# Performance work log

Hardware: AMD Instinct MI355X
Metric: run time of the kernel (lower is better)

The kernel has to match this reference:

```python
import jax, jax.numpy as jnp
import numpy as np


def setup_inputs() -> dict:
    key = jax.random.key(0)
    k1, k2 = jax.random.split(key)
    B, L, D = 8, 4096, 1024
    hidden_states = jax.random.normal(k1, (B, L, D), dtype=jnp.float32)
    token_mask = jax.random.bernoulli(k2, 0.5, (B, L))
    return {"hidden_states": hidden_states, "token_mask": token_mask}


def reference(hidden_states, token_mask):
    """Compact hidden states at masked positions, left-packed and zero-padded.

    Returns (chunked: (B, M, D), counts: (B,)) where M = max tokens per row.
    Vectorized: prefix-sum over the mask gives per-row scatter destinations;
    masked-out positions are routed to a scratch slot M that is sliced off.
    """
    B, L, D = hidden_states.shape
    counts = token_mask.sum(axis=1).astype(jnp.int32)  # (B,)
    M = int(jnp.max(counts))  # data-dependent pad width (eager, matches .item())
    if M == 0:
        return hidden_states[:, :0, :], counts
    # destination index within each row: 0..count-1 for kept tokens, M for dropped
    dest = jnp.where(token_mask, jnp.cumsum(token_mask, axis=1) - 1, M)  # (B, L)
    b_idx = jnp.arange(B)[:, None]  # (B, 1)
    out = jnp.zeros((B, M + 1, D), hidden_states.dtype)
    out = out.at[b_idx, dest].set(hidden_states)  # single fused scatter
    chunked = out[:, :M, :]  # drop scratch slot
    return chunked, counts
```

## Files before the change

kernel.cpp:

```cpp
#include <hip/hip_runtime.h>
#include <hip/hip_bf16.h>


__global__ void scan_kernel(const int* __restrict__ mask,
                            int* __restrict__ src_idx,
                            int* __restrict__ counts_ws,
                            float* __restrict__ counts_out,
                            int L, int M) {
    const int b = blockIdx.x;
    const int t = threadIdx.x;
    const int nthreads = blockDim.x;
    const int per = L / nthreads;
    const int* row = mask + (size_t)b * L;
    const int base = t * per;

    int s = 0;
    for (int i = 0; i < per; ++i) s += (row[base + i] != 0);

    __shared__ int sums[256];
    sums[t] = s;
    __syncthreads();

    for (int off = 1; off < nthreads; off <<= 1) {
        int v = (t >= off) ? sums[t - off] : 0;
        __syncthreads();
        sums[t] += v;
        __syncthreads();
    }

    const int total = sums[nthreads - 1];
    int prefix = (t == 0) ? 0 : sums[t - 1];

    int* srow = src_idx + (size_t)b * M;
    for (int i = 0; i < per; ++i) {
        if (row[base + i] != 0) {
            srow[prefix] = base + i;
            ++prefix;
        }
    }

    if (t == 0) {
        counts_ws[b] = total;
        counts_out[b] = (float)total;
    }
}

__global__ void pack_kernel(const float4* __restrict__ hidden,
                            const int* __restrict__ src_idx,
                            const int* __restrict__ counts,
                            float4* __restrict__ out,
                            int L, int M, int D4) {
    const int m = blockIdx.x;
    const int b = blockIdx.y;
    const size_t orow = ((size_t)b * M + m) * D4;

    if (m < counts[b]) {
        const int l = src_idx[(size_t)b * M + m];
        const size_t irow = ((size_t)b * L + l) * D4;
        for (int t = threadIdx.x; t < D4; t += blockDim.x)
            out[orow + t] = hidden[irow + t];
    } else {
        const float4 z = make_float4(0.f, 0.f, 0.f, 0.f);
        for (int t = threadIdx.x; t < D4; t += blockDim.x)
            out[orow + t] = z;
    }
}

extern "C" void kernel_launch(void* const* d_in, const int* in_sizes, int n_in,
                              void* d_out, int out_size, void* d_ws, size_t ws_size,
                              hipStream_t stream) {
    const int B = 8;
    const int BL = in_sizes[1];
    const int D  = in_sizes[0] / BL;
    const int L  = BL / B;
    const int M  = (out_size - B) / (B * D);

    const float* hidden = (const float*)d_in[0];
    const int*   mask   = (const int*)d_in[1];
    float*       out    = (float*)d_out;

    int* counts_ws = (int*)d_ws;
    int* src_idx   = (int*)d_ws + 64;

    float* counts_out = out + (size_t)B * M * D;

    scan_kernel<<<B, 256, 0, stream>>>(mask, src_idx, counts_ws, counts_out, L, M);

    if (M > 0) {
        dim3 grid(M, B);
        pack_kernel<<<grid, 256, 0, stream>>>((const float4*)hidden, src_idx,
                                              counts_ws, (float4*)out, L, M, D / 4);
    }
}
```

Before: 205.1 us.

## Use wave-shuffle scan with 1024 threads and grid-stride persistent pack kernel

```diff
diff --git a/kernel.cpp b/kernel.cpp
--- a/kernel.cpp
+++ b/kernel.cpp
@@ -2,67 +2,73 @@
 #include <hip/hip_bf16.h>
 
 
-__global__ void scan_kernel(const int* __restrict__ mask,
-                            int* __restrict__ src_idx,
-                            int* __restrict__ counts_ws,
-                            float* __restrict__ counts_out,
-                            int L, int M) {
+__global__ __launch_bounds__(1024) void scan_kernel(
+        const int* __restrict__ mask,
+        int* __restrict__ src_idx,
+        int* __restrict__ counts_ws,
+        float* __restrict__ counts_out,
+        int L, int M) {
     const int b = blockIdx.x;
     const int t = threadIdx.x;
-    const int nthreads = blockDim.x;
-    const int per = L / nthreads;
-    const int* row = mask + (size_t)b * L;
-    const int base = t * per;
+    const int lane = t & 63;
+    const int wid  = t >> 6;
+    const int base = t * 4;
 
-    int s = 0;
-    for (int i = 0; i < per; ++i) s += (row[base + i] != 0);
+    const int4 v = *(const int4*)(mask + (size_t)b * L + base);
+    const int m0 = (v.x != 0), m1 = (v.y != 0), m2 = (v.z != 0), m3 = (v.w != 0);
+    const int s = m0 + m1 + m2 + m3;
 
-    __shared__ int sums[256];
-    sums[t] = s;
+    int incl = s;
+    #pragma unroll
+    for (int off = 1; off < 64; off <<= 1) {
+        int up = __shfl_up(incl, off, 64);
+        if (lane >= off) incl += up;
+    }
+
+    __shared__ int wsum[16];
+    __shared__ int wexc[17];
+    if (lane == 63) wsum[wid] = incl;
+    __syncthreads();
+    if (t == 0) {
+        int acc = 0;
+        #pragma unroll
+        for (int w = 0; w < 16; ++w) { wexc[w] = acc; acc += wsum[w]; }
+        wexc[16] = acc;
+        counts_ws[b] = acc;
+        counts_out[b] = (float)acc;
+    }
     __syncthreads();
 
-    for (int off = 1; off < nthreads; off <<= 1) {
-        int v = (t >= off) ? sums[t - off] : 0;
-        __syncthreads();
-        sums[t] += v;
-        __syncthreads();
-    }
-
-    const int total = sums[nthreads - 1];
-    int prefix = (t == 0) ? 0 : sums[t - 1];
+    int prefix = wexc[wid] + (incl - s);
 
     int* srow = src_idx + (size_t)b * M;
-    for (int i = 0; i < per; ++i) {
-        if (row[base + i] != 0) {
-            srow[prefix] = base + i;
-            ++prefix;
-        }
-    }
-
-    if (t == 0) {
-        counts_ws[b] = total;
-        counts_out[b] = (float)total;
-    }
+    if (m0) srow[prefix++] = base + 0;
+    if (m1) srow[prefix++] = base + 1;
+    if (m2) srow[prefix++] = base + 2;
+    if (m3) srow[prefix]   = base + 3;
 }
 
-__global__ void pack_kernel(const float4* __restrict__ hidden,
-                            const int* __restrict__ src_idx,
-                            const int* __restrict__ counts,
-                            float4* __restrict__ out,
-                            int L, int M, int D4) {
-    const int m = blockIdx.x;
-    const int b = blockIdx.y;
-    const size_t orow = ((size_t)b * M + m) * D4;
-
-    if (m < counts[b]) {
-        const int l = src_idx[(size_t)b * M + m];
-        const size_t irow = ((size_t)b * L + l) * D4;
-        for (int t = threadIdx.x; t < D4; t += blockDim.x)
-            out[orow + t] = hidden[irow + t];
-    } else {
-        const float4 z = make_float4(0.f, 0.f, 0.f, 0.f);
-        for (int t = threadIdx.x; t < D4; t += blockDim.x)
-            out[orow + t] = z;
+__global__ __launch_bounds__(256) void pack_kernel(
+        const float4* __restrict__ hidden,
+        const int* __restrict__ src_idx,
+        const int* __restrict__ counts,
+        float4* __restrict__ out,
+        int L, int M, int D4, int nrows) {
+    const int t = threadIdx.x;
+    for (int r = blockIdx.x; r < nrows; r += gridDim.x) {
+        const int b = r / M;
+        const int m = r - b * M;
+        const size_t orow = (size_t)r * D4;
+        if (m < counts[b]) {
+            const int l = src_idx[r];
+            const size_t irow = ((size_t)b * L + l) * D4;
+            for (int i = t; i < D4; i += blockDim.x)
+                out[orow + i] = hidden[irow + i];
+        } else {
+            const float4 z = make_float4(0.f, 0.f, 0.f, 0.f);
+            for (int i = t; i < D4; i += blockDim.x)
+                out[orow + i] = z;
+        }
     }
 }
 
@@ -84,11 +90,13 @@
 
     float* counts_out = out + (size_t)B * M * D;
 
-    scan_kernel<<<B, 256, 0, stream>>>(mask, src_idx, counts_ws, counts_out, L, M);
+    scan_kernel<<<B, 1024, 0, stream>>>(mask, src_idx, counts_ws, counts_out, L, M);
 
     if (M > 0) {
-        dim3 grid(M, B);
+        const int nrows = B * M;
+        int grid = nrows < 2048 ? nrows : 2048;
         pack_kernel<<<grid, 256, 0, stream>>>((const float4*)hidden, src_idx,
-                                              counts_ws, (float4*)out, L, M, D / 4);
+                                              counts_ws, (float4*)out, L, M,
+                                              D / 4, nrows);
     }
 }
```

Result: no change. 203.7 us (-0.7%).
